# Performance work log

Hardware: AMD Instinct MI355X
Metric: run time of the kernel (lower is better)

Reference implementation:

```python
import jax, jax.numpy as jnp
import numpy as np

SQRT2 = 1.41421356237
BASE_SCALE = 0.001
CDF_X = 10.0


def erf_poly(x):
    # Abramowitz-Stegun polynomial erf, exactly as the torch source
    sign = jnp.where(x > 0, 1.0, -1.0)  # torch: (x > 0) * 2 - 1
    x = jnp.abs(x)
    a1, a2, a3, a4, a5 = 0.254829592, -0.284496736, 1.421413741, -1.453152027, 1.061405429
    p = 0.3275911
    t = 1.0 / (1.0 + p * x)
    y = 1.0 - ((((a5 * t + a4) * t + a3) * t + a2) * t + a1) * t * jnp.exp(-x * x)
    return sign * y


def rot6d_to_rotmat(x):
    # Zhou et al. 6D rotation: Gram-Schmidt two columns, cross for third
    a1, a2 = x[..., :3], x[..., 3:6]
    b1 = a1 / jnp.linalg.norm(a1, axis=-1, keepdims=True)
    b2 = a2 - jnp.sum(b1 * a2, axis=-1, keepdims=True) * b1
    b2 = b2 / jnp.linalg.norm(b2, axis=-1, keepdims=True)
    b3 = jnp.cross(b1, b2)
    return jnp.stack([b1, b2, b3], axis=-1)  # columns b1,b2,b3 -> [..., 3, 3]


def setup_inputs() -> dict:
    key = jax.random.key(0)
    k1, k2, k3, k4 = jax.random.split(key, 4)
    R, B, G = 65536, 24, 4
    return {
        "w2ls": jax.random.normal(k1, (R, B, 4, 4), dtype=jnp.float32),
        "rays_o": jax.random.normal(k2, (R, 3), dtype=jnp.float32),
        "rays_d": jax.random.normal(k3, (R, 3), dtype=jnp.float32),
        "Gs": jax.random.normal(k4, (B, G, 13), dtype=jnp.float32),
        "N_unique": 1,
    }


def reference(w2ls, rays_o, rays_d, Gs, N_unique):
    # Gs-derived quantities are detached in the original get_1D_gaussians
    Gs = jax.lax.stop_gradient(Gs)
    R = rays_o.shape[0]
    dt = rays_o.dtype

    origins = jnp.concatenate([rays_o, jnp.ones((R, 1), dt)], axis=1)      # [r,4]
    dirs = jnp.concatenate([rays_d, jnp.zeros((R, 1), dt)], axis=1)        # [r,4]
    o = jnp.einsum('rbij,rj->rbi', w2ls, origins)[..., :3]                 # [r,b,3]
    n = jnp.einsum('rbij,rj->rbi', w2ls, dirs)[..., :3]                    # [r,b,3]

    G_mu = Gs[..., 0:3]                                                    # [b,g,3]
    G_std = jnp.abs(Gs[..., 3:6]) + BASE_SCALE                             # [b,g,3]
    G_R = rot6d_to_rotmat(Gs[..., 6:12])                                   # [b,g,3,3]
    G_c = jnp.abs(Gs[..., 12])                                             # [b,g]

    # S = diag(1/std); SR = S @ R scales rows of R
    SR = G_R / G_std[..., None]                                            # [b,g,3,3]
    Sn1 = jnp.einsum('bgki,bgkj->bgij', SR, SR)                            # R^T S^2 R

    mu_d_o = G_mu[None] - o[:, :, None, :]                                 # [r,b,g,3]
    nSn = jnp.einsum('rbi,bgij,rbj->rbg', n, Sn1, n)                       # n^T Sn1 n
    sigma_bar_sqr = 1.0 / nSn                                              # [r,b,g]
    mu_bar = jnp.einsum('rbi,bgij,rbgj->rbg', n, Sn1, mu_d_o) * sigma_bar_sqr
    quad = jnp.einsum('rbgi,bgij,rbgj->rbg', mu_d_o, Sn1, mu_d_o)

    densities = G_c[None] * jnp.exp(-0.5 * (quad - mu_bar ** 2 / sigma_bar_sqr))
    means = mu_bar
    sigmas = jnp.sqrt(sigma_bar_sqr)

    # soft density filter (weights computed on detached means)
    w = jax.nn.sigmoid(100.0 * jax.lax.stop_gradient(means) - 1.0)
    densities = densities * w

    # gaussian1d_cdf at x = 10.0, then shadow map: sum over all (bone, gaussian)
    cdf = densities * 0.5 * (1.0 + erf_poly((CDF_X - means) / (sigmas * SQRT2)))
    shadow_map = jnp.exp(-jnp.sum(cdf, axis=(1, 2)))                       # [r]
    return shadow_map
```

## Files before the change

### kernel.cpp

```cpp
#include <hip/hip_runtime.h>
#include <math.h>


#define NB 24
#define NG 4
#define BASE_SCALE 0.001f

template <int CTRL>
__device__ __forceinline__ float dpp_f(float x) {
    int r = __builtin_amdgcn_update_dpp(0, __float_as_int(x), CTRL, 0xF, 0xF, true);
    return __int_as_float(r);
}

__device__ __forceinline__ float frcp(float x) { return __builtin_amdgcn_rcpf(x); }

__global__ __launch_bounds__(256, 4) void gauss_vis_kernel(
    const float* __restrict__ w2ls,
    const float* __restrict__ rays_o,
    const float* __restrict__ rays_d,
    const float* __restrict__ Gs,
    float* __restrict__ out,
    int R)
{
    __shared__ float4 P[NB * NG * 3];

    const int tid = threadIdx.x;
    const int gid = blockIdx.x * 256 + tid;
    const int ray0 = gid >> 3;
    const int ray = ray0 < R ? ray0 : (R - 1);
    const int oct = tid & 7;
    const int sub = oct & 3;
    const int half = oct >> 2;

    const float4* __restrict__ Wp =
        (const float4*)w2ls + ((size_t)ray * (NB * 4) + half * 4 + sub);
    float4 M[12];
#pragma unroll
    for (int k = 0; k < 12; ++k) M[k] = Wp[k * 8];

    const float rox = rays_o[ray * 3 + 0];
    const float roy = rays_o[ray * 3 + 1];
    const float roz = rays_o[ray * 3 + 2];
    const float rdx = rays_d[ray * 3 + 0];
    const float rdy = rays_d[ray * 3 + 1];
    const float rdz = rays_d[ray * 3 + 2];

    if (tid < NB * NG) {
        const float* gp = Gs + tid * 13;
        float mu0 = gp[0], mu1 = gp[1], mu2 = gp[2];
        float s0 = fabsf(gp[3]) + BASE_SCALE;
        float s1 = fabsf(gp[4]) + BASE_SCALE;
        float s2 = fabsf(gp[5]) + BASE_SCALE;
        float ax = gp[6], ay = gp[7], az = gp[8];
        float bx = gp[9], by = gp[10], bz = gp[11];
        float c = fabsf(gp[12]);
        float inv1 = 1.0f / sqrtf(ax * ax + ay * ay + az * az);
        float b1x = ax * inv1, b1y = ay * inv1, b1z = az * inv1;
        float dot = b1x * bx + b1y * by + b1z * bz;
        float t2x = bx - dot * b1x, t2y = by - dot * b1y, t2z = bz - dot * b1z;
        float inv2 = 1.0f / sqrtf(t2x * t2x + t2y * t2y + t2z * t2z);
        float b2x = t2x * inv2, b2y = t2y * inv2, b2z = t2z * inv2;
        float b3x = b1y * b2z - b1z * b2y;
        float b3y = b1z * b2x - b1x * b2z;
        float b3z = b1x * b2y - b1y * b2x;
        float w0 = 1.0f / (s0 * s0), w1 = 1.0f / (s1 * s1), w2 = 1.0f / (s2 * s2);
        float s00 = b1x * b1x * w0 + b1y * b1y * w1 + b1z * b1z * w2;
        float s01 = b1x * b2x * w0 + b1y * b2y * w1 + b1z * b2z * w2;
        float s02 = b1x * b3x * w0 + b1y * b3y * w1 + b1z * b3z * w2;
        float s11 = b2x * b2x * w0 + b2y * b2y * w1 + b2z * b2z * w2;
        float s12 = b2x * b3x * w0 + b2y * b3y * w1 + b2z * b3z * w2;
        float s22 = b3x * b3x * w0 + b3y * b3y * w1 + b3z * b3z * w2;
        P[tid * 3 + 0] = make_float4(s00, s01, s02, s11);
        P[tid * 3 + 1] = make_float4(s12, s22, mu0, mu1);
        P[tid * 3 + 2] = make_float4(mu2, c, 0.f, 0.f);
    }
    __syncthreads();

    const int pi0 = (half * NG + sub) * 3;

    float sum = 0.f;
#pragma unroll
    for (int k = 0; k < 12; ++k) {
        const float4 Mk = M[k];
        float o_s = Mk.x * rox + Mk.y * roy + Mk.z * roz + Mk.w;
        float n_s = Mk.x * rdx + Mk.y * rdy + Mk.z * rdz;
        float o0 = dpp_f<0x00>(o_s), o1 = dpp_f<0x55>(o_s), o2 = dpp_f<0xAA>(o_s);
        float n0 = dpp_f<0x00>(n_s), n1 = dpp_f<0x55>(n_s), n2 = dpp_f<0xAA>(n_s);

        int pi = pi0 + k * 24;
        float4 p0 = P[pi + 0];
        float4 p1 = P[pi + 1];
        float4 p2 = P[pi + 2];
        float s00 = p0.x, s01 = p0.y, s02 = p0.z, s11 = p0.w;
        float s12 = p1.x, s22 = p1.y;
        float d0 = p1.z - o0, d1 = p1.w - o1, d2 = p2.x - o2;
        float c = p2.y;

        float v0 = s00 * n0 + s01 * n1 + s02 * n2;
        float v1 = s01 * n0 + s11 * n1 + s12 * n2;
        float v2 = s02 * n0 + s12 * n1 + s22 * n2;
        float nSn = v0 * n0 + v1 * n1 + v2 * n2;
        float nSd = v0 * d0 + v1 * d1 + v2 * d2;
        float q0 = s00 * d0 + s01 * d1 + s02 * d2;
        float q1 = s01 * d0 + s11 * d1 + s12 * d2;
        float q2 = s02 * d0 + s12 * d1 + s22 * d2;
        float quad = q0 * d0 + q1 * d1 + q2 * d2;

        float rn = frcp(nSn);
        float mean = nSd * rn;
        float expo = -0.5f * (quad - nSd * nSd * rn);
        float dens = c * __expf(expo);
        float wsig = frcp(1.f + __expf(1.f - 100.f * mean));
        float arg = (10.f - mean) * __builtin_amdgcn_sqrtf(nSn * 0.5f);
        float sgn = arg > 0.f ? 1.f : -1.f;
        float xa = fabsf(arg);
        float t = frcp(1.f + 0.3275911f * xa);
        float poly = ((((1.061405429f * t - 1.453152027f) * t + 1.421413741f) * t
                       - 0.284496736f) * t + 0.254829592f) * t;
        float erf = sgn * (1.f - poly * __expf(-xa * xa));

        sum += dens * wsig * 0.5f * (1.f + erf);
    }

    sum += dpp_f<0xB1>(sum);
    sum += dpp_f<0x4E>(sum);
    sum += __shfl_xor(sum, 4, 64);
    if (oct == 0 && ray0 < R) out[ray0] = __expf(-sum);
}

extern "C" void kernel_launch(void* const* d_in, const int* in_sizes, int n_in,
                              void* d_out, int out_size, void* d_ws, size_t ws_size,
                              hipStream_t stream) {
    const float* w2ls   = (const float*)d_in[0];
    const float* rays_o = (const float*)d_in[1];
    const float* rays_d = (const float*)d_in[2];
    const float* Gs     = (const float*)d_in[3];
    float* out = (float*)d_out;

    const int R = in_sizes[1] / 3;
    const int threads = 256;
    const long long total = (long long)R * 8;
    const int blocks = (int)((total + threads - 1) / threads);
    gauss_vis_kernel<<<blocks, threads, 0, stream>>>(w2ls, rays_o, rays_d, Gs, out, R);
}
```

Before: 27.81 us.

## Use persistent grid-stride loop with double-buffered w2ls prefetch

Replaces the one-ray-group-per-thread launch with a fixed grid of 512 blocks that loop over rays in grid-stride fashion. The next ray's 12 float4 matrix loads are issued into a second register buffer while the current ray is being computed, so memory latency overlaps with the math. It also amortises the per-block Gaussian precompute and shared-memory setup over many rays. The cost is doubled register use for the two buffers, which is why the launch-bounds occupancy hint drops to 2, and fewer resident waves may hide latency less well.

Measured after the change: 32.23 us. 1.16x slower.

```diff
diff --git a/kernel.cpp b/kernel.cpp
--- a/kernel.cpp
+++ b/kernel.cpp
@@ -14,7 +14,7 @@
 
 __device__ __forceinline__ float frcp(float x) { return __builtin_amdgcn_rcpf(x); }
 
-__global__ __launch_bounds__(256, 4) void gauss_vis_kernel(
+__global__ __launch_bounds__(256, 2) void gauss_vis_kernel(
     const float* __restrict__ w2ls,
     const float* __restrict__ rays_o,
     const float* __restrict__ rays_d,
@@ -25,25 +25,13 @@
     __shared__ float4 P[NB * NG * 3];
 
     const int tid = threadIdx.x;
-    const int gid = blockIdx.x * 256 + tid;
-    const int ray0 = gid >> 3;
-    const int ray = ray0 < R ? ray0 : (R - 1);
     const int oct = tid & 7;
     const int sub = oct & 3;
     const int half = oct >> 2;
+    const int slot = (blockIdx.x * 256 + tid) >> 3;
+    const int strideR = (gridDim.x * 256) >> 3;
 
-    const float4* __restrict__ Wp =
-        (const float4*)w2ls + ((size_t)ray * (NB * 4) + half * 4 + sub);
-    float4 M[12];
-#pragma unroll
-    for (int k = 0; k < 12; ++k) M[k] = Wp[k * 8];
-
-    const float rox = rays_o[ray * 3 + 0];
-    const float roy = rays_o[ray * 3 + 1];
-    const float roz = rays_o[ray * 3 + 2];
-    const float rdx = rays_d[ray * 3 + 0];
-    const float rdy = rays_d[ray * 3 + 1];
-    const float rdz = rays_d[ray * 3 + 2];
+    const float4* __restrict__ Wv = (const float4*)w2ls;
 
     if (tid < NB * NG) {
         const float* gp = Gs + tid * 13;
@@ -78,54 +66,82 @@
 
     const int pi0 = (half * NG + sub) * 3;
 
-    float sum = 0.f;
+    auto loadray = [&](float4 (&buf)[12], int r) {
+        int rc = r < R ? r : (R - 1);
+        const float4* __restrict__ p = Wv + ((size_t)rc * (NB * 4) + half * 4 + sub);
 #pragma unroll
-    for (int k = 0; k < 12; ++k) {
-        const float4 Mk = M[k];
-        float o_s = Mk.x * rox + Mk.y * roy + Mk.z * roz + Mk.w;
-        float n_s = Mk.x * rdx + Mk.y * rdy + Mk.z * rdz;
-        float o0 = dpp_f<0x00>(o_s), o1 = dpp_f<0x55>(o_s), o2 = dpp_f<0xAA>(o_s);
-        float n0 = dpp_f<0x00>(n_s), n1 = dpp_f<0x55>(n_s), n2 = dpp_f<0xAA>(n_s);
+        for (int k = 0; k < 12; ++k) buf[k] = p[k * 8];
+    };
 
-        int pi = pi0 + k * 24;
-        float4 p0 = P[pi + 0];
-        float4 p1 = P[pi + 1];
-        float4 p2 = P[pi + 2];
-        float s00 = p0.x, s01 = p0.y, s02 = p0.z, s11 = p0.w;
-        float s12 = p1.x, s22 = p1.y;
-        float d0 = p1.z - o0, d1 = p1.w - o1, d2 = p2.x - o2;
-        float c = p2.y;
+    auto computeray = [&](const float4 (&buf)[12], int r) {
+        if (r >= R) return;
+        float rox = rays_o[r * 3 + 0], roy = rays_o[r * 3 + 1], roz = rays_o[r * 3 + 2];
+        float rdx = rays_d[r * 3 + 0], rdy = rays_d[r * 3 + 1], rdz = rays_d[r * 3 + 2];
+        float sum = 0.f;
+#pragma unroll
+        for (int k = 0; k < 12; ++k) {
+            const float4 Mk = buf[k];
+            float o_s = Mk.x * rox + Mk.y * roy + Mk.z * roz + Mk.w;
+            float n_s = Mk.x * rdx + Mk.y * rdy + Mk.z * rdz;
+            float o0 = dpp_f<0x00>(o_s), o1 = dpp_f<0x55>(o_s), o2 = dpp_f<0xAA>(o_s);
+            float n0 = dpp_f<0x00>(n_s), n1 = dpp_f<0x55>(n_s), n2 = dpp_f<0xAA>(n_s);
 
-        float v0 = s00 * n0 + s01 * n1 + s02 * n2;
-        float v1 = s01 * n0 + s11 * n1 + s12 * n2;
-        float v2 = s02 * n0 + s12 * n1 + s22 * n2;
-        float nSn = v0 * n0 + v1 * n1 + v2 * n2;
-        float nSd = v0 * d0 + v1 * d1 + v2 * d2;
-        float q0 = s00 * d0 + s01 * d1 + s02 * d2;
-        float q1 = s01 * d0 + s11 * d1 + s12 * d2;
-        float q2 = s02 * d0 + s12 * d1 + s22 * d2;
-        float quad = q0 * d0 + q1 * d1 + q2 * d2;
+            int pi = pi0 + k * 24;
+            float4 p0 = P[pi + 0];
+            float4 p1 = P[pi + 1];
+            float4 p2 = P[pi + 2];
+            float s00 = p0.x, s01 = p0.y, s02 = p0.z, s11 = p0.w;
+            float s12 = p1.x, s22 = p1.y;
+            float d0 = p1.z - o0, d1 = p1.w - o1, d2 = p2.x - o2;
+            float c = p2.y;
 
-        float rn = frcp(nSn);
-        float mean = nSd * rn;
-        float expo = -0.5f * (quad - nSd * nSd * rn);
-        float dens = c * __expf(expo);
-        float wsig = frcp(1.f + __expf(1.f - 100.f * mean));
-        float arg = (10.f - mean) * __builtin_amdgcn_sqrtf(nSn * 0.5f);
-        float sgn = arg > 0.f ? 1.f : -1.f;
-        float xa = fabsf(arg);
-        float t = frcp(1.f + 0.3275911f * xa);
-        float poly = ((((1.061405429f * t - 1.453152027f) * t + 1.421413741f) * t
-                       - 0.284496736f) * t + 0.254829592f) * t;
-        float erf = sgn * (1.f - poly * __expf(-xa * xa));
+            float v0 = s00 * n0 + s01 * n1 + s02 * n2;
+            float v1 = s01 * n0 + s11 * n1 + s12 * n2;
+            float v2 = s02 * n0 + s12 * n1 + s22 * n2;
+            float nSn = v0 * n0 + v1 * n1 + v2 * n2;
+            float nSd = v0 * d0 + v1 * d1 + v2 * d2;
+            float q0 = s00 * d0 + s01 * d1 + s02 * d2;
+            float q1 = s01 * d0 + s11 * d1 + s12 * d2;
+            float q2 = s02 * d0 + s12 * d1 + s22 * d2;
+            float quad = q0 * d0 + q1 * d1 + q2 * d2;
 
-        sum += dens * wsig * 0.5f * (1.f + erf);
+            float rn = frcp(nSn);
+            float mean = nSd * rn;
+            float expo = -0.5f * (quad - nSd * nSd * rn);
+            float dens = c * __expf(expo);
+            float wsig = frcp(1.f + __expf(1.f - 100.f * mean));
+            float arg = (10.f - mean) * __builtin_amdgcn_sqrtf(nSn * 0.5f);
+            float sgn = arg > 0.f ? 1.f : -1.f;
+            float xa = fabsf(arg);
+            float t = frcp(1.f + 0.3275911f * xa);
+            float poly = ((((1.061405429f * t - 1.453152027f) * t + 1.421413741f) * t
+                           - 0.284496736f) * t + 0.254829592f) * t;
+            float erf = sgn * (1.f - poly * __expf(-xa * xa));
+
+            sum += dens * wsig * 0.5f * (1.f + erf);
+        }
+        sum += dpp_f<0xB1>(sum);
+        sum += dpp_f<0x4E>(sum);
+        sum += __shfl_xor(sum, 4, 64);
+        if (oct == 0) out[r] = __expf(-sum);
+    };
+
+    float4 A[12], Bf[12];
+    int ray = slot;
+    loadray(A, ray);
+    while (true) {
+        int nray = ray + strideR;
+        loadray(Bf, nray);
+        computeray(A, ray);
+        ray = nray;
+        if (ray >= R) break;
+
+        nray = ray + strideR;
+        loadray(A, nray);
+        computeray(Bf, ray);
+        ray = nray;
+        if (ray >= R) break;
     }
-
-    sum += dpp_f<0xB1>(sum);
-    sum += dpp_f<0x4E>(sum);
-    sum += __shfl_xor(sum, 4, 64);
-    if (oct == 0 && ray0 < R) out[ray0] = __expf(-sum);
 }
 
 extern "C" void kernel_launch(void* const* d_in, const int* in_sizes, int n_in,
@@ -139,7 +155,8 @@
 
     const int R = in_sizes[1] / 3;
     const int threads = 256;
-    const long long total = (long long)R * 8;
-    const int blocks = (int)((total + threads - 1) / threads);
+    int blocks = 512;
+    const long long slots = (long long)blocks * threads / 8;
+    if (slots > R) blocks = (int)((R * 8LL + threads - 1) / threads);
     gauss_vis_kernel<<<blocks, threads, 0, stream>>>(w2ls, rays_o, rays_d, Gs, out, R);
 }
```

## Stage w2ls through per-wave LDS tile with fully coalesced global loads

Applied to the files above, without the earlier changes.

Each wave now loads its contiguous 8-ray window of w2ls with lane-consecutive float4 loads into a shared-memory tile, then reads per-lane matrices from LDS. The loads now start after the Gs precompute barrier rather than before it. The goal is to replace the earlier strided per-lane loads (stride of 8 float4) with fully coalesced accesses. In exchange it adds 48KB of LDS per block plus an extra LDS round-trip, and it drops the occupancy hint from launch bounds. The added LDS may limit the number of resident blocks.

Result: slower. 31.50 us (+13.3%).

```diff
diff --git a/kernel.cpp b/kernel.cpp
--- a/kernel.cpp
+++ b/kernel.cpp
@@ -14,7 +14,7 @@
 
 __device__ __forceinline__ float frcp(float x) { return __builtin_amdgcn_rcpf(x); }
 
-__global__ __launch_bounds__(256, 4) void gauss_vis_kernel(
+__global__ __launch_bounds__(256) void gauss_vis_kernel(
     const float* __restrict__ w2ls,
     const float* __restrict__ rays_o,
     const float* __restrict__ rays_d,
@@ -23,27 +23,11 @@
     int R)
 {
     __shared__ float4 P[NB * NG * 3];
+    __shared__ float4 tile[4][768];
 
     const int tid = threadIdx.x;
-    const int gid = blockIdx.x * 256 + tid;
-    const int ray0 = gid >> 3;
-    const int ray = ray0 < R ? ray0 : (R - 1);
-    const int oct = tid & 7;
-    const int sub = oct & 3;
-    const int half = oct >> 2;
-
-    const float4* __restrict__ Wp =
-        (const float4*)w2ls + ((size_t)ray * (NB * 4) + half * 4 + sub);
-    float4 M[12];
-#pragma unroll
-    for (int k = 0; k < 12; ++k) M[k] = Wp[k * 8];
-
-    const float rox = rays_o[ray * 3 + 0];
-    const float roy = rays_o[ray * 3 + 1];
-    const float roz = rays_o[ray * 3 + 2];
-    const float rdx = rays_d[ray * 3 + 0];
-    const float rdy = rays_d[ray * 3 + 1];
-    const float rdz = rays_d[ray * 3 + 2];
+    const int wave = tid >> 6;
+    const int lane = tid & 63;
 
     if (tid < NB * NG) {
         const float* gp = Gs + tid * 13;
@@ -76,12 +60,45 @@
     }
     __syncthreads();
 
+    const int gid = blockIdx.x * 256 + tid;
+    const int ray0 = gid >> 3;
+    const int ray = ray0 < R ? ray0 : (R - 1);
+    const int wray0 = (blockIdx.x * 256 + wave * 64) >> 3;
+    const size_t window = (size_t)wray0 * 96;
+    const size_t maxf4 = (size_t)R * 96;
+    const float4* __restrict__ Wv = (const float4*)w2ls;
+
+    float4 buf[12];
+#pragma unroll
+    for (int k = 0; k < 12; ++k) {
+        size_t idx = window + (size_t)(k * 64 + lane);
+        if (idx >= maxf4) idx = maxf4 - 1;
+        buf[k] = Wv[idx];
+    }
+#pragma unroll
+    for (int k = 0; k < 12; ++k) tile[wave][k * 64 + lane] = buf[k];
+    asm volatile("s_waitcnt lgkmcnt(0)" ::: "memory");
+    __builtin_amdgcn_sched_barrier(0);
+
+    const int o8 = lane & 7;
+    const int octet = lane >> 3;
+    const int sub = o8 & 3;
+    const int half = o8 >> 2;
     const int pi0 = (half * NG + sub) * 3;
+
+    const float rox = rays_o[ray * 3 + 0];
+    const float roy = rays_o[ray * 3 + 1];
+    const float roz = rays_o[ray * 3 + 2];
+    const float rdx = rays_d[ray * 3 + 0];
+    const float rdy = rays_d[ray * 3 + 1];
+    const float rdz = rays_d[ray * 3 + 2];
+
+    const float4* __restrict__ tbase = &tile[wave][octet * 96 + half * 4 + sub];
 
     float sum = 0.f;
 #pragma unroll
     for (int k = 0; k < 12; ++k) {
-        const float4 Mk = M[k];
+        const float4 Mk = tbase[k * 8];
         float o_s = Mk.x * rox + Mk.y * roy + Mk.z * roz + Mk.w;
         float n_s = Mk.x * rdx + Mk.y * rdy + Mk.z * rdz;
         float o0 = dpp_f<0x00>(o_s), o1 = dpp_f<0x55>(o_s), o2 = dpp_f<0xAA>(o_s);
@@ -125,7 +142,7 @@
     sum += dpp_f<0xB1>(sum);
     sum += dpp_f<0x4E>(sum);
     sum += __shfl_xor(sum, 4, 64);
-    if (oct == 0 && ray0 < R) out[ray0] = __expf(-sum);
+    if (o8 == 0 && ray0 < R) out[ray0] = __expf(-sum);
 }
 
 extern "C" void kernel_launch(void* const* d_in, const int* in_sizes, int n_in,
```
